# Performance work log

Measured on AMD Instinct MI355X. Metric: run time of the kernel, lower is better.

## Reference

```python
import jax, jax.numpy as jnp
import numpy as np

H = 512  # hidden_size


def setup_inputs() -> dict:
    key = jax.random.key(0)
    ks = jax.random.split(key, 12)
    B, E, S, V = 64, 512, 400, 50000
    s = 1.0 / np.sqrt(H)
    inp = {
        'embedded': jax.random.normal(ks[0], (B, E), jnp.float32),
        'hidden': jax.random.normal(ks[1], (1, B, H), jnp.float32),
        'encoder_states': jax.random.normal(ks[2], (S, B, H), jnp.float32),
        # GRU params (PyTorch layout: gates ordered r,z,n)
        'w_ih': jax.random.uniform(ks[3], (3 * H, E), jnp.float32, -s, s),
        'w_hh': jax.random.uniform(ks[4], (3 * H, H), jnp.float32, -s, s),
        'b_ih': jax.random.uniform(ks[5], (3 * H,), jnp.float32, -s, s),
        'b_hh': jax.random.uniform(ks[6], (3 * H,), jnp.float32, -s, s),
        # nn.Bilinear(H, H, 1)
        'bilin_w': jax.random.uniform(ks[7], (1, H, H), jnp.float32, -s, s),
        'bilin_b': jax.random.uniform(ks[8], (1,), jnp.float32, -s, s),
        # out: Linear(2H, V)
        'out_w': jax.random.uniform(ks[9], (V, 2 * H), jnp.float32, -1.0 / np.sqrt(2 * H), 1.0 / np.sqrt(2 * H)),
        'out_b': jax.random.uniform(ks[10], (V,), jnp.float32, -1.0 / np.sqrt(2 * H), 1.0 / np.sqrt(2 * H)),
    }
    return inp


def reference(embedded, hidden, encoder_states, w_ih, w_hh, b_ih, b_hh,
              bilin_w, bilin_b, out_w, out_b):
    h0 = hidden[0]                                   # [B, H]
    # --- single-step GRU cell (PyTorch gate order r, z, n) ---
    gi = embedded @ w_ih.T + b_ih                    # [B, 3H]
    gh = h0 @ w_hh.T + b_hh                          # [B, 3H]
    r = jax.nn.sigmoid(gi[:, :H] + gh[:, :H])
    z = jax.nn.sigmoid(gi[:, H:2 * H] + gh[:, H:2 * H])
    n = jnp.tanh(gi[:, 2 * H:] + r * gh[:, 2 * H:])
    h_new = (1.0 - z) * n + z * h0                   # [B, H]
    # --- bilinear attention: energy[s,b] = h_new[b] @ W @ enc[s,b] + bias ---
    tmp = h_new @ bilin_w[0]                         # [B, H]
    energy = jnp.einsum('bh,sbh->sb', tmp, encoder_states) + bilin_b[0]  # [S, B]
    attn = jax.nn.softmax(energy, axis=0)            # softmax over source positions
    context = jnp.einsum('sb,sbh->bh', attn, encoder_states)             # [B, H]
    combined = jnp.concatenate([h_new, context], axis=1)                 # [B, 2H]
    logits = combined @ out_w.T + out_b              # [B, V]
    logp = jax.nn.log_softmax(logits, axis=1)
    return logp, h_new[None], attn[:, :, None]
```

## Files before the change

### kernel.cpp

```cpp
#include <hip/hip_runtime.h>
#include <math.h>

static constexpr int H = 512;
static constexpr int B = 64;

typedef __bf16 bf16x8 __attribute__((ext_vector_type(8)));
typedef __bf16 bf16x4 __attribute__((ext_vector_type(4)));
typedef float f32x4 __attribute__((ext_vector_type(4)));

__global__ __launch_bounds__(256) void gemm_mfma_nt(
    const float* __restrict__ A,
    const float* __restrict__ W,
    const float* __restrict__ bias,
    float* __restrict__ C,
    int K, int N, int ldc)
{
    __shared__ __bf16 As[2][64 * 64];
    __shared__ __bf16 Ws[2][64 * 64];

    const int tid  = threadIdx.x;
    const int lane = tid & 63;
    const int wv   = tid >> 6;
    const int n0   = blockIdx.x * 64;

    const int lrow = tid >> 2;
    const int lq   = tid & 3;

    int wrow = n0 + lrow;
    if (wrow > N - 1) wrow = N - 1;
    const float* Aptr = A + (size_t)lrow * K + lq * 16;
    const float* Wptr = W + (size_t)wrow * K + lq * 16;

    f32x4 acc[4] = {};

    float4 ra[4], rw[4];
    #pragma unroll
    for (int i = 0; i < 4; ++i) {
        ra[i] = *(const float4*)(Aptr + 4 * i);
        rw[i] = *(const float4*)(Wptr + 4 * i);
    }

    const int ln = lane & 15;
    const int lk = (lane >> 4) << 3;
    const int NT = K >> 6;

    for (int t = 0; t < NT; ++t) {
        __bf16* a_s = As[t & 1];
        __bf16* w_s = Ws[t & 1];
        #pragma unroll
        for (int i = 0; i < 4; ++i) {
            const int off = ((lrow << 6) + lq * 16 + 4 * i) ^ ((lrow & 7) << 3);
            bf16x4 va = { (__bf16)ra[i].x, (__bf16)ra[i].y, (__bf16)ra[i].z, (__bf16)ra[i].w };
            bf16x4 vw = { (__bf16)rw[i].x, (__bf16)rw[i].y, (__bf16)rw[i].z, (__bf16)rw[i].w };
            *(bf16x4*)&a_s[off] = va;
            *(bf16x4*)&w_s[off] = vw;
        }
        __syncthreads();
        if (t + 1 < NT) {
            const float* Ap = Aptr + (t + 1) * 64;
            const float* Wp = Wptr + (t + 1) * 64;
            #pragma unroll
            for (int i = 0; i < 4; ++i) {
                ra[i] = *(const float4*)(Ap + 4 * i);
                rw[i] = *(const float4*)(Wp + 4 * i);
            }
        }
        bf16x8 bfrag[2];
        #pragma unroll
        for (int ks = 0; ks < 2; ++ks) {
            const int row = wv * 16 + ln;
            const int off = ((row << 6) + ks * 32 + lk) ^ ((row & 7) << 3);
            bfrag[ks] = *(bf16x8*)&w_s[off];
        }
        #pragma unroll
        for (int m = 0; m < 4; ++m) {
            const int row = m * 16 + ln;
            #pragma unroll
            for (int ks = 0; ks < 2; ++ks) {
                const int off = ((row << 6) + ks * 32 + lk) ^ ((row & 7) << 3);
                bf16x8 afrag = *(bf16x8*)&a_s[off];
                acc[m] = __builtin_amdgcn_mfma_f32_16x16x32_bf16(afrag, bfrag[ks], acc[m], 0, 0, 0);
            }
        }
    }

    const int col = n0 + wv * 16 + ln;
    if (col < N) {
        const float bv = bias ? bias[col] : 0.f;
        #pragma unroll
        for (int m = 0; m < 4; ++m) {
            const int rbase = m * 16 + (lane >> 4) * 4;
            #pragma unroll
            for (int j = 0; j < 4; ++j)
                C[(size_t)(rbase + j) * ldc + col] = acc[m][j] + bv;
        }
    }
}

__global__ __launch_bounds__(256) void gemm_a64_kn(
    const float* __restrict__ A, const float* __restrict__ W,
    float* __restrict__ C, int K, int N, int ldc)
{
    __shared__ float As[64][68];
    __shared__ float Bs[64][68];
    const int tid = threadIdx.x;
    const int n0 = blockIdx.x * 64;
    const int tv = tid & 15;
    const int tb = tid >> 4;
    const int lrow = tid >> 2;
    const int lk0  = (tid & 3) * 16;

    float acc[4][4] = {{0.f, 0.f, 0.f, 0.f}};

    for (int kc = 0; kc < K; kc += 64) {
        #pragma unroll
        for (int i = 0; i < 4; ++i) {
            const float4 a = *(const float4*)(A + (size_t)lrow * K + kc + lk0 + 4 * i);
            As[lk0 + 4 * i + 0][lrow] = a.x;
            As[lk0 + 4 * i + 1][lrow] = a.y;
            As[lk0 + 4 * i + 2][lrow] = a.z;
            As[lk0 + 4 * i + 3][lrow] = a.w;
        }
        {
            const int v  = tid & 63;
            const int kg = tid >> 6;
            #pragma unroll
            for (int i = 0; i < 16; ++i) {
                const int kk = kg * 16 + i;
                Bs[kk][v] = (n0 + v < N) ? W[(size_t)(kc + kk) * N + n0 + v] : 0.f;
            }
        }
        __syncthreads();
        #pragma unroll 16
        for (int kk = 0; kk < 64; ++kk) {
            const float4 a = *(const float4*)&As[kk][tb * 4];
            const float4 b = *(const float4*)&Bs[kk][tv * 4];
            acc[0][0] += a.x * b.x; acc[0][1] += a.x * b.y; acc[0][2] += a.x * b.z; acc[0][3] += a.x * b.w;
            acc[1][0] += a.y * b.x; acc[1][1] += a.y * b.y; acc[1][2] += a.y * b.z; acc[1][3] += a.y * b.w;
            acc[2][0] += a.z * b.x; acc[2][1] += a.z * b.y; acc[2][2] += a.z * b.z; acc[2][3] += a.z * b.w;
            acc[3][0] += a.w * b.x; acc[3][1] += a.w * b.y; acc[3][2] += a.w * b.z; acc[3][3] += a.w * b.w;
        }
        __syncthreads();
    }
    #pragma unroll
    for (int i = 0; i < 4; ++i) {
        const int bb = tb * 4 + i;
        #pragma unroll
        for (int j = 0; j < 4; ++j) {
            const int n = n0 + tv * 4 + j;
            if (n < N) C[(size_t)bb * ldc + n] = acc[i][j];
        }
    }
}

__global__ __launch_bounds__(512) void gru_gates(
    const float* __restrict__ gi, const float* __restrict__ gh,
    const float* __restrict__ h0, float* __restrict__ hnew,
    float* __restrict__ combined)
{
    const int b = blockIdx.x;
    const int h = threadIdx.x;
    const size_t o = (size_t)b * 3 * H;
    const float r = 1.f / (1.f + expf(-(gi[o + h] + gh[o + h])));
    const float z = 1.f / (1.f + expf(-(gi[o + H + h] + gh[o + H + h])));
    const float n = tanhf(gi[o + 2 * H + h] + r * gh[o + 2 * H + h]);
    const float hn = (1.f - z) * n + z * h0[(size_t)b * H + h];
    hnew[(size_t)b * H + h] = hn;
    combined[(size_t)b * 2 * H + h] = hn;
}

__global__ __launch_bounds__(256) void energy_k(
    const float* __restrict__ tmp, const float* __restrict__ enc,
    const float* __restrict__ bilin_b, float* __restrict__ energy, int S)
{
    const int gw = (int)((blockIdx.x * 256 + threadIdx.x) >> 6);
    const int lane = threadIdx.x & 63;
    if (gw >= S * B) return;
    const int s = gw >> 6;
    const int b = gw & 63;
    const float* e = enc + ((size_t)s * B + b) * H;
    const float* t = tmp + (size_t)b * H;
    const int k0 = lane * 8;
    const float4 e0 = *(const float4*)(e + k0);
    const float4 e1 = *(const float4*)(e + k0 + 4);
    const float4 t0 = *(const float4*)(t + k0);
    const float4 t1 = *(const float4*)(t + k0 + 4);
    float p = e0.x * t0.x + e0.y * t0.y + e0.z * t0.z + e0.w * t0.w
            + e1.x * t1.x + e1.y * t1.y + e1.z * t1.z + e1.w * t1.w;
    #pragma unroll
    for (int off = 32; off; off >>= 1) p += __shfl_down(p, off);
    if (lane == 0) energy[(size_t)s * B + b] = p + bilin_b[0];
}

__global__ __launch_bounds__(128) void softmax_s(
    const float* __restrict__ energy, float* __restrict__ attn, int S)
{
    const int b = blockIdx.x;
    const int t = threadIdx.x;
    __shared__ float w0[2], w1[2];
    float m = -1e30f;
    for (int s = t; s < S; s += 128) m = fmaxf(m, energy[(size_t)s * B + b]);
    #pragma unroll
    for (int off = 32; off; off >>= 1) m = fmaxf(m, __shfl_xor(m, off));
    if ((t & 63) == 0) w0[t >> 6] = m;
    __syncthreads();
    m = fmaxf(w0[0], w0[1]);
    float sum = 0.f;
    for (int s = t; s < S; s += 128) sum += expf(energy[(size_t)s * B + b] - m);
    #pragma unroll
    for (int off = 32; off; off >>= 1) sum += __shfl_xor(sum, off);
    if ((t & 63) == 0) w1[t >> 6] = sum;
    __syncthreads();
    const float inv = 1.f / (w1[0] + w1[1]);
    for (int s = t; s < S; s += 128)
        attn[(size_t)s * B + b] = expf(energy[(size_t)s * B + b] - m) * inv;
}

static constexpr int CSP = 8;
__global__ __launch_bounds__(512) void context_part(
    const float* __restrict__ attn, const float* __restrict__ enc,
    float* __restrict__ part, int S, int chunk)
{
    const int b = blockIdx.x;
    const int p = blockIdx.y;
    const int h = threadIdx.x;
    const int s0 = p * chunk;
    int s1 = s0 + chunk; if (s1 > S) s1 = S;
    __shared__ float a_s[128];
    if (h < s1 - s0) a_s[h] = attn[(size_t)(s0 + h) * B + b];
    __syncthreads();
    float c = 0.f;
    const float* e = enc + ((size_t)s0 * B + b) * H + h;
    for (int s = s0; s < s1; ++s, e += (size_t)B * H)
        c += a_s[s - s0] * (*e);
    part[((size_t)p * B + b) * H + h] = c;
}

__global__ __launch_bounds__(512) void context_reduce(
    const float* __restrict__ part, float* __restrict__ combined)
{
    const int b = blockIdx.x;
    const int h = threadIdx.x;
    float c = 0.f;
    #pragma unroll
    for (int p = 0; p < CSP; ++p) c += part[((size_t)p * B + b) * H + h];
    combined[(size_t)b * 2 * H + H + h] = c;
}

static constexpr int LSP = 16;
__global__ __launch_bounds__(256) void lsm_part(
    const float* __restrict__ logits, float* __restrict__ pm,
    float* __restrict__ ps, int V)
{
    const int b = blockIdx.x;
    const int p = blockIdx.y;
    const int t = threadIdx.x;
    const int V4 = V >> 2;
    const int chunk = (V4 + LSP - 1) / LSP;
    const int i0 = p * chunk;
    int i1 = i0 + chunk; if (i1 > V4) i1 = V4;
    const float4* row = (const float4*)(logits + (size_t)b * V);
    __shared__ float sm[4], ss[4];

    float m = -1e30f;
    for (int i = i0 + t; i < i1; i += 256) {
        const float4 v = row[i];
        m = fmaxf(fmaxf(fmaxf(m, v.x), v.y), fmaxf(v.z, v.w));
    }
    #pragma unroll
    for (int off = 32; off; off >>= 1) m = fmaxf(m, __shfl_xor(m, off));
    if ((t & 63) == 0) sm[t >> 6] = m;
    __syncthreads();
    m = fmaxf(fmaxf(sm[0], sm[1]), fmaxf(sm[2], sm[3]));

    float s = 0.f;
    for (int i = i0 + t; i < i1; i += 256) {
        const float4 v = row[i];
        s += expf(v.x - m) + expf(v.y - m) + expf(v.z - m) + expf(v.w - m);
    }
    #pragma unroll
    for (int off = 32; off; off >>= 1) s += __shfl_xor(s, off);
    if ((t & 63) == 0) ss[t >> 6] = s;
    __syncthreads();
    if (t == 0) {
        pm[b * LSP + p] = m;
        ps[b * LSP + p] = ss[0] + ss[1] + ss[2] + ss[3];
    }
}

__global__ __launch_bounds__(64) void lsm_combine(
    const float* __restrict__ pm, const float* __restrict__ ps,
    float* __restrict__ c)
{
    const int b = blockIdx.x;
    const int l = threadIdx.x;
    float m = (l < LSP) ? pm[b * LSP + l] : -1e30f;
    float mm = m;
    #pragma unroll
    for (int off = 32; off; off >>= 1) mm = fmaxf(mm, __shfl_xor(mm, off));
    float s = (l < LSP) ? ps[b * LSP + l] * expf(m - mm) : 0.f;
    #pragma unroll
    for (int off = 32; off; off >>= 1) s += __shfl_xor(s, off);
    if (l == 0) c[b] = mm + logf(s);
}

__global__ __launch_bounds__(256) void lsm_apply(
    float* __restrict__ logits, const float* __restrict__ c, int V)
{
    const int b = blockIdx.y;
    const int i = blockIdx.x * 256 + threadIdx.x;
    const int V4 = V >> 2;
    if (i >= V4) return;
    float4* row = (float4*)(logits + (size_t)b * V);
    float4 v = row[i];
    const float cb = c[b];
    v.x -= cb; v.y -= cb; v.z -= cb; v.w -= cb;
    row[i] = v;
}

extern "C" void kernel_launch(void* const* d_in, const int* in_sizes, int n_in,
                              void* d_out, int out_size, void* d_ws, size_t ws_size,
                              hipStream_t stream)
{
    const float* embedded = (const float*)d_in[0];
    const float* hidden   = (const float*)d_in[1];
    const float* enc      = (const float*)d_in[2];
    const float* w_ih     = (const float*)d_in[3];
    const float* w_hh     = (const float*)d_in[4];
    const float* b_ih     = (const float*)d_in[5];
    const float* b_hh     = (const float*)d_in[6];
    const float* bilin_w  = (const float*)d_in[7];
    const float* bilin_b  = (const float*)d_in[8];
    const float* out_w    = (const float*)d_in[9];
    const float* out_b    = (const float*)d_in[10];
    float* out = (float*)d_out;

    const int E = in_sizes[0] / B;
    const int S = in_sizes[2] / (B * H);
    const int V = in_sizes[9] / (2 * H);

    float* logp = out;
    float* hnew = out + (size_t)B * V;
    float* attn = hnew + (size_t)B * H;

    float* ws       = (float*)d_ws;
    float* gi       = ws;
    float* gh       = gi + (size_t)B * 3 * H;
    float* tmp      = gh + (size_t)B * 3 * H;
    float* energy   = tmp + (size_t)B * H;
    float* combined = energy + (size_t)S * B;
    float* part     = combined + (size_t)B * 2 * H;
    float* pm       = part + (size_t)CSP * B * H;
    float* ps       = pm + (size_t)B * LSP;
    float* cb       = ps + (size_t)B * LSP;

    gemm_mfma_nt<<<(3 * H) / 64, 256, 0, stream>>>(embedded, w_ih, b_ih, gi, E, 3 * H, 3 * H);
    gemm_mfma_nt<<<(3 * H) / 64, 256, 0, stream>>>(hidden, w_hh, b_hh, gh, H, 3 * H, 3 * H);

    gru_gates<<<B, H, 0, stream>>>(gi, gh, hidden, hnew, combined);

    gemm_a64_kn<<<H / 64, 256, 0, stream>>>(hnew, bilin_w, tmp, H, H, H);

    energy_k<<<(S * B + 3) / 4, 256, 0, stream>>>(tmp, enc, bilin_b, energy, S);

    softmax_s<<<B, 128, 0, stream>>>(energy, attn, S);

    const int chunk = (S + CSP - 1) / CSP;
    context_part<<<dim3(B, CSP), 512, 0, stream>>>(attn, enc, part, S, chunk);
    context_reduce<<<B, 512, 0, stream>>>(part, combined);

    gemm_mfma_nt<<<(V + 63) / 64, 256, 0, stream>>>(combined, out_w, out_b, logp, 2 * H, V, V);

    lsm_part<<<dim3(B, LSP), 256, 0, stream>>>(logp, pm, ps, V);
    lsm_combine<<<B, 64, 0, stream>>>(pm, ps, cb);
    lsm_apply<<<dim3((V / 4 + 255) / 256, B), 256, 0, stream>>>(logp, cb, V);
}
```

Baseline: 178.9 us.

## Stream output projection weights directly into MFMA with pre-converted bf16 activations

The gru_gates and context_reduce kernels now write the combined activation as bf16. A new gemm_stream_nt kernel loads out_w rows straight from global memory into MFMA B-fragments without staging them in LDS or calling __syncthreads, and reads the bf16 A operand directly from global memory and cache. This aims to cut LDS traffic and barrier overhead in the large vocabulary GEMM, which is bound by weight bandwidth. In exchange it gives up double buffering and makes uncoalesced 32-byte strided loads per lane, relying on occupancy to hide latency.

```diff
diff --git a/kernel.cpp b/kernel.cpp
--- a/kernel.cpp
+++ b/kernel.cpp
@@ -3,16 +3,18 @@
 
 static constexpr int H = 512;
 static constexpr int B = 64;
+static constexpr int CSP = 8;
+static constexpr int LSP = 16;
 
 typedef __bf16 bf16x8 __attribute__((ext_vector_type(8)));
 typedef __bf16 bf16x4 __attribute__((ext_vector_type(4)));
 typedef float f32x4 __attribute__((ext_vector_type(4)));
 
+__device__ __forceinline__ float sigmoidf_(float x) { return 1.f / (1.f + expf(-x)); }
+
 __global__ __launch_bounds__(256) void gemm_mfma_nt(
-    const float* __restrict__ A,
-    const float* __restrict__ W,
-    const float* __restrict__ bias,
-    float* __restrict__ C,
+    const float* __restrict__ A, const float* __restrict__ W,
+    const float* __restrict__ bias, float* __restrict__ C,
     int K, int N, int ldc)
 {
     __shared__ __bf16 As[2][64 * 64];
@@ -22,7 +24,6 @@
     const int lane = tid & 63;
     const int wv   = tid >> 6;
     const int n0   = blockIdx.x * 64;
-
     const int lrow = tid >> 2;
     const int lq   = tid & 3;
 
@@ -32,7 +33,6 @@
     const float* Wptr = W + (size_t)wrow * K + lq * 16;
 
     f32x4 acc[4] = {};
-
     float4 ra[4], rw[4];
     #pragma unroll
     for (int i = 0; i < 4; ++i) {
@@ -50,10 +50,8 @@
         #pragma unroll
         for (int i = 0; i < 4; ++i) {
             const int off = ((lrow << 6) + lq * 16 + 4 * i) ^ ((lrow & 7) << 3);
-            bf16x4 va = { (__bf16)ra[i].x, (__bf16)ra[i].y, (__bf16)ra[i].z, (__bf16)ra[i].w };
-            bf16x4 vw = { (__bf16)rw[i].x, (__bf16)rw[i].y, (__bf16)rw[i].z, (__bf16)rw[i].w };
-            *(bf16x4*)&a_s[off] = va;
-            *(bf16x4*)&w_s[off] = vw;
+            *(bf16x4*)&a_s[off] = bf16x4{ (__bf16)ra[i].x, (__bf16)ra[i].y, (__bf16)ra[i].z, (__bf16)ra[i].w };
+            *(bf16x4*)&w_s[off] = bf16x4{ (__bf16)rw[i].x, (__bf16)rw[i].y, (__bf16)rw[i].z, (__bf16)rw[i].w };
         }
         __syncthreads();
         if (t + 1 < NT) {
@@ -97,6 +95,70 @@
     }
 }
 
+__global__ __launch_bounds__(256, 4) void gemm_stream_nt(
+    const __bf16* __restrict__ Ab,
+    const float* __restrict__ W,
+    const float* __restrict__ bias,
+    float* __restrict__ C, int K, int N, int ldc)
+{
+    const int lane = threadIdx.x & 63;
+    const int wv   = threadIdx.x >> 6;
+    const int n0   = blockIdx.x * 64 + wv * 16;
+    const int ln   = lane & 15;
+    const int lk8  = (lane >> 4) << 3;
+
+    int wr = n0 + ln;
+    if (wr > N - 1) wr = N - 1;
+    const float*  wp = W  + (size_t)wr * K + lk8;
+    const __bf16* ap = Ab + (size_t)ln * K + lk8;
+
+    f32x4 acc[4] = {};
+    const int NKS = K >> 5;
+
+    #pragma unroll 2
+    for (int ks = 0; ks < NKS; ++ks) {
+        const float4 w0 = *(const float4*)(wp);
+        const float4 w1 = *(const float4*)(wp + 4);
+        wp += 32;
+        const bf16x8 bw = { (__bf16)w0.x, (__bf16)w0.y, (__bf16)w0.z, (__bf16)w0.w,
+                            (__bf16)w1.x, (__bf16)w1.y, (__bf16)w1.z, (__bf16)w1.w };
+        #pragma unroll
+        for (int m = 0; m < 4; ++m) {
+            const bf16x8 af = *(const bf16x8*)(ap + (size_t)m * 16 * K);
+            acc[m] = __builtin_amdgcn_mfma_f32_16x16x32_bf16(af, bw, acc[m], 0, 0, 0);
+        }
+        ap += 32;
+    }
+
+    const int col = n0 + ln;
+    if (col < N) {
+        const float bv = bias[col];
+        #pragma unroll
+        for (int m = 0; m < 4; ++m) {
+            const int rbase = m * 16 + (lane >> 4) * 4;
+            #pragma unroll
+            for (int j = 0; j < 4; ++j)
+                C[(size_t)(rbase + j) * ldc + col] = acc[m][j] + bv;
+        }
+    }
+}
+
+__global__ __launch_bounds__(512) void gru_gates(
+    const float* __restrict__ gi, const float* __restrict__ gh,
+    const float* __restrict__ h0, float* __restrict__ hnew,
+    __bf16* __restrict__ cbf)
+{
+    const int b = blockIdx.x;
+    const int h = threadIdx.x;
+    const size_t o = (size_t)b * 3 * H;
+    const float r = sigmoidf_(gi[o + h] + gh[o + h]);
+    const float z = sigmoidf_(gi[o + H + h] + gh[o + H + h]);
+    const float n = tanhf(gi[o + 2 * H + h] + r * gh[o + 2 * H + h]);
+    const float hn = (1.f - z) * n + z * h0[(size_t)b * H + h];
+    hnew[(size_t)b * H + h] = hn;
+    cbf[(size_t)b * 2 * H + h] = (__bf16)hn;
+}
+
 __global__ __launch_bounds__(256) void gemm_a64_kn(
     const float* __restrict__ A, const float* __restrict__ W,
     float* __restrict__ C, int K, int N, int ldc)
@@ -151,22 +213,6 @@
             if (n < N) C[(size_t)bb * ldc + n] = acc[i][j];
         }
     }
-}
-
-__global__ __launch_bounds__(512) void gru_gates(
-    const float* __restrict__ gi, const float* __restrict__ gh,
-    const float* __restrict__ h0, float* __restrict__ hnew,
-    float* __restrict__ combined)
-{
-    const int b = blockIdx.x;
-    const int h = threadIdx.x;
-    const size_t o = (size_t)b * 3 * H;
-    const float r = 1.f / (1.f + expf(-(gi[o + h] + gh[o + h])));
-    const float z = 1.f / (1.f + expf(-(gi[o + H + h] + gh[o + H + h])));
-    const float n = tanhf(gi[o + 2 * H + h] + r * gh[o + 2 * H + h]);
-    const float hn = (1.f - z) * n + z * h0[(size_t)b * H + h];
-    hnew[(size_t)b * H + h] = hn;
-    combined[(size_t)b * 2 * H + h] = hn;
 }
 
 __global__ __launch_bounds__(256) void energy_k(
@@ -216,7 +262,6 @@
         attn[(size_t)s * B + b] = expf(energy[(size_t)s * B + b] - m) * inv;
 }
 
-static constexpr int CSP = 8;
 __global__ __launch_bounds__(512) void context_part(
     const float* __restrict__ attn, const float* __restrict__ enc,
     float* __restrict__ part, int S, int chunk)
@@ -237,17 +282,16 @@
 }
 
 __global__ __launch_bounds__(512) void context_reduce(
-    const float* __restrict__ part, float* __restrict__ combined)
+    const float* __restrict__ part, __bf16* __restrict__ cbf)
 {
     const int b = blockIdx.x;
     const int h = threadIdx.x;
     float c = 0.f;
     #pragma unroll
     for (int p = 0; p < CSP; ++p) c += part[((size_t)p * B + b) * H + h];
-    combined[(size_t)b * 2 * H + H + h] = c;
-}
-
-static constexpr int LSP = 16;
+    cbf[(size_t)b * 2 * H + H + h] = (__bf16)c;
+}
+
 __global__ __launch_bounds__(256) void lsm_part(
     const float* __restrict__ logits, float* __restrict__ pm,
     float* __restrict__ ps, int V)
@@ -343,21 +387,21 @@
     float* hnew = out + (size_t)B * V;
     float* attn = hnew + (size_t)B * H;
 
-    float* ws       = (float*)d_ws;
-    float* gi       = ws;
-    float* gh       = gi + (size_t)B * 3 * H;
-    float* tmp      = gh + (size_t)B * 3 * H;
-    float* energy   = tmp + (size_t)B * H;
-    float* combined = energy + (size_t)S * B;
-    float* part     = combined + (size_t)B * 2 * H;
-    float* pm       = part + (size_t)CSP * B * H;
-    float* ps       = pm + (size_t)B * LSP;
-    float* cb       = ps + (size_t)B * LSP;
+    float* ws     = (float*)d_ws;
+    float* gi     = ws;
+    float* gh     = gi + (size_t)B * 3 * H;
+    float* tmp    = gh + (size_t)B * 3 * H;
+    float* energy = tmp + (size_t)B * H;
+    float* part   = energy + (size_t)S * B;
+    float* pm     = part + (size_t)CSP * B * H;
+    float* ps     = pm + (size_t)B * LSP;
+    float* cb     = ps + (size_t)B * LSP;
+    __bf16* cbf   = (__bf16*)(cb + 64);
 
     gemm_mfma_nt<<<(3 * H) / 64, 256, 0, stream>>>(embedded, w_ih, b_ih, gi, E, 3 * H, 3 * H);
     gemm_mfma_nt<<<(3 * H) / 64, 256, 0, stream>>>(hidden, w_hh, b_hh, gh, H, 3 * H, 3 * H);
 
-    gru_gates<<<B, H, 0, stream>>>(gi, gh, hidden, hnew, combined);
+    gru_gates<<<B, H, 0, stream>>>(gi, gh, hidden, hnew, cbf);
 
     gemm_a64_kn<<<H / 64, 256, 0, stream>>>(hnew, bilin_w, tmp, H, H, H);
 
@@ -367,9 +411,9 @@
 
     const int chunk = (S + CSP - 1) / CSP;
     context_part<<<dim3(B, CSP), 512, 0, stream>>>(attn, enc, part, S, chunk);
-    context_reduce<<<B, 512, 0, stream>>>(part, combined);
-
-    gemm_mfma_nt<<<(V + 63) / 64, 256, 0, stream>>>(combined, out_w, out_b, logp, 2 * H, V, V);
+    context_reduce<<<B, 512, 0, stream>>>(part, cbf);
+
+    gemm_stream_nt<<<(V + 63) / 64, 256, 0, stream>>>(cbf, out_w, out_b, logp, 2 * H, V, V);
 
     lsm_part<<<dim3(B, LSP), 256, 0, stream>>>(logp, pm, ps, V);
     lsm_combine<<<B, 64, 0, stream>>>(pm, ps, cb);
```

After: 218.5 us. +22.2%, slower.
